# Optimization experiments

Measured on AMD Instinct MI355X. Metric: run time of the kernel, lower is better.

## Reference

```python
import jax, jax.numpy as jnp
import numpy as np

EMB = 768
HEADS = 8
HEAD_DIM = EMB // HEADS
SCALE = HEAD_DIM ** -0.5


def setup_inputs() -> dict:
    key = jax.random.key(0)
    ks = jax.random.split(key, 9)
    s = EMB ** -0.5
    return {
        "x": jax.random.normal(ks[0], (2, 4096, EMB), dtype=jnp.float32),
        "Wq": jax.random.normal(ks[1], (EMB, EMB), dtype=jnp.float32) * s,
        "bq": jax.random.normal(ks[2], (EMB,), dtype=jnp.float32) * 0.02,
        "Wk": jax.random.normal(ks[3], (EMB, EMB), dtype=jnp.float32) * s,
        "bk": jax.random.normal(ks[4], (EMB,), dtype=jnp.float32) * 0.02,
        "Wv": jax.random.normal(ks[5], (EMB, EMB), dtype=jnp.float32) * s,
        "bv": jax.random.normal(ks[6], (EMB,), dtype=jnp.float32) * 0.02,
        "Wo": jax.random.normal(ks[7], (EMB, EMB), dtype=jnp.float32) * s,
        "bo": jax.random.normal(ks[8], (EMB,), dtype=jnp.float32) * 0.02,
    }


def reference(x, Wq, bq, Wk, bk, Wv, bv, Wo, bo):
    b, n, _ = x.shape
    def split_heads(t):  # [b, n, emb] -> [b, h, n, d]
        return t.reshape(b, n, HEADS, HEAD_DIM).transpose(0, 2, 1, 3)
    q = split_heads(x @ Wq + bq)
    k = split_heads(x @ Wk + bk)
    v = split_heads(x @ Wv + bv)
    scores = jnp.einsum('bhqd,bhkd->bhqk', q, k)
    # NOTE: faithful to source — softmax first, THEN multiply by scale.
    attn = jax.nn.softmax(scores, axis=-1) * SCALE
    out = jnp.einsum('bhqk,bhkd->bhqd', attn, v)
    out = out.transpose(0, 2, 1, 3).reshape(b, n, EMB)
    return out @ Wo + bo
```

## Files before the change

### kernel.cpp

```cpp
#include <hip/hip_runtime.h>
#include <hip/hip_fp16.h>


typedef _Float16 half8 __attribute__((ext_vector_type(8)));
typedef _Float16 half4 __attribute__((ext_vector_type(4)));
typedef float   float4_ __attribute__((ext_vector_type(4)));
typedef float   f32x16 __attribute__((ext_vector_type(16)));

#define SCALE 0.102062072615966f
#define LOG2E 1.44269504088896340736f

__device__ __forceinline__ float4_ mfma16(half8 a, half8 b, float4_ c) {
    return __builtin_amdgcn_mfma_f32_16x16x32_f16(a, b, c, 0, 0, 0);
}
__device__ __forceinline__ f32x16 mfma32(half8 a, half8 b, f32x16 c) {
    return __builtin_amdgcn_mfma_f32_32x32x16_f16(a, b, c, 0, 0, 0);
}
__device__ __forceinline__ void gload16(const _Float16* g, _Float16* l) {
    __builtin_amdgcn_global_load_lds(
        (const __attribute__((address_space(1))) void*)g,
        (__attribute__((address_space(3))) void*)l, 16, 0, 0);
}


__global__ void cast_x(const float* __restrict__ x, _Float16* __restrict__ xb) {
    int i = blockIdx.x * 256 + threadIdx.x;
    float4_ v = ((const float4_*)x)[i];
    half4 h = { (_Float16)v[0], (_Float16)v[1], (_Float16)v[2], (_Float16)v[3] };
    ((half4*)xb)[i] = h;
}

__global__ void prep_w(const float* __restrict__ Wq, const float* __restrict__ Wk,
                       const float* __restrict__ Wv, const float* __restrict__ Wo,
                       _Float16* __restrict__ wqkv, _Float16* __restrict__ wot) {
    __shared__ float tile[64][65];
    const int bid = blockIdx.x;
    const int mat = bid / 144, rem = bid % 144;
    const int kt = rem / 12, ct = rem % 12;
    const float* W = (mat == 0) ? Wq : (mat == 1) ? Wk : (mat == 2) ? Wv : Wo;
    const int k0 = kt * 64, c0 = ct * 64;
    const int t = threadIdx.x;
    const int lr = t >> 4, lc = (t & 15) * 4;
    #pragma unroll
    for (int i = 0; i < 4; ++i) {
        float4_ v = *(const float4_*)(W + (size_t)(k0 + i * 16 + lr) * 768 + c0 + lc);
        tile[i * 16 + lr][lc + 0] = v[0];
        tile[i * 16 + lr][lc + 1] = v[1];
        tile[i * 16 + lr][lc + 2] = v[2];
        tile[i * 16 + lr][lc + 3] = v[3];
    }
    __syncthreads();
    const int cr = t >> 2, kq = (t & 3) * 16;
    _Float16* dst = (mat < 3) ? (wqkv + ((size_t)(mat * 768 + c0 + cr)) * 768 + k0 + kq)
                              : (wot  + ((size_t)(c0 + cr)) * 768 + k0 + kq);
    half8 h0, h1;
    #pragma unroll
    for (int j = 0; j < 8; ++j) {
        h0[j] = (_Float16)tile[kq + j][cr];
        h1[j] = (_Float16)tile[kq + 8 + j][cr];
    }
    *(half8*)dst = h0;
    *(half8*)(dst + 8) = h1;
}

__global__ void prep_bias(const float* __restrict__ bq, const float* __restrict__ bk,
                          const float* __restrict__ bv, float* __restrict__ bqkv) {
    int i = blockIdx.x * 256 + threadIdx.x;
    float v = (i < 768) ? bq[i] : (i < 1536) ? bk[i - 768] : bv[i - 1536];
    bqkv[i] = v;
}

__global__ __launch_bounds__(256, 2) void gemm_kernel(
    const _Float16* __restrict__ A, const _Float16* __restrict__ Bt,
    const float* __restrict__ bias, int mode,
    _Float16* __restrict__ Qo, _Float16* __restrict__ Ko, _Float16* __restrict__ Vto,
    float* __restrict__ out)
{
    __shared__ alignas(16) _Float16 Af[16 * 512];
    __shared__ alignas(16) _Float16 Bf[16 * 512];
    const int tid = threadIdx.x;
    const int lane = tid & 63, w = tid >> 6;
    const int wm = w >> 1, wn = w & 1;
    const int l15 = lane & 15, l4 = lane >> 4;
    const int m0 = blockIdx.y * 128;
    const int n0 = blockIdx.x * 128;

    const _Float16* gs[8];
    _Float16* ld[8];
    #pragma unroll
    for (int i = 0; i < 8; ++i) {
        int f = (w & 1) * 8 + i;
        int rg = f >> 1, kc = f & 1;
        int r0 = ((w < 2) ? m0 : n0) + rg * 16;
        gs[i] = ((w < 2) ? A : Bt) + (size_t)(r0 + l15) * 768 + kc * 32 + l4 * 8;
        ld[i] = ((w < 2) ? Af : Bf) + f * 512;
    }

    float4_ acc[4][4] = {};

    for (int k0 = 0; k0 < 768; k0 += 64) {
        #pragma unroll
        for (int i = 0; i < 8; ++i)
            gload16(gs[i] + k0, ld[i]);
        __syncthreads();
        #pragma unroll
        for (int kc = 0; kc < 2; ++kc) {
            half8 bfr[4];
            #pragma unroll
            for (int nt = 0; nt < 4; ++nt)
                bfr[nt] = *(const half8*)(Bf + (size_t)(((wn * 4 + nt) * 2 + kc) * 512 + lane * 8));
            #pragma unroll
            for (int mt = 0; mt < 4; ++mt) {
                half8 afr = *(const half8*)(Af + (size_t)(((wm * 4 + mt) * 2 + kc) * 512 + lane * 8));
                #pragma unroll
                for (int nt = 0; nt < 4; ++nt)
                    acc[mt][nt] = mfma16(afr, bfr[nt], acc[mt][nt]);
            }
        }
        __syncthreads();
    }

    #pragma unroll
    for (int mt = 0; mt < 4; ++mt)
    #pragma unroll
    for (int nt = 0; nt < 4; ++nt) {
        int gc = n0 + wn * 64 + nt * 16 + l15;
        float bv_ = bias[gc];
        #pragma unroll
        for (int r = 0; r < 4; ++r) {
            int gm = m0 + wm * 64 + mt * 16 + l4 * 4 + r;
            float val = acc[mt][nt][r] + bv_;
            if (mode == 1) {
                out[(size_t)gm * 768 + gc] = val;
            } else {
                int b = gm >> 12, n = gm & 4095;
                if (gc < 768) {
                    int h = gc / 96, d = gc % 96;
                    Qo[(((size_t)(b * 8 + h)) * 4096 + n) * 96 + d] = (_Float16)(val * LOG2E);
                } else if (gc < 1536) {
                    int c = gc - 768, h = c / 96, d = c % 96;
                    int bh = b * 8 + h;
                    size_t idx = (((size_t)bh * 128 + (n >> 5)) * 6 + (d >> 4)) * 512
                               + (size_t)((d >> 3) & 1) * 256 + (size_t)(n & 31) * 8 + (d & 7);
                    Ko[idx] = (_Float16)val;
                } else {
                    int c = gc - 1536, h = c / 96, d = c % 96;
                    int bh = b * 8 + h;
                    size_t idx = (((size_t)bh * 64 + (n >> 6)) * 12 + ((n >> 4) & 3) * 3 + (d >> 5)) * 512
                               + (size_t)((n >> 3) & 1) * 256 + (size_t)(d & 31) * 8 + (n & 7);
                    Vto[idx] = (_Float16)val;
                }
            }
        }
    }
}

__global__ __launch_bounds__(256, 2) void attn_kernel(
    const _Float16* __restrict__ Q, const _Float16* __restrict__ Kf,
    const _Float16* __restrict__ Vf, _Float16* __restrict__ AO)
{
    __shared__ alignas(16) _Float16 kvbuf[2][24 * 512];
    __shared__ float tab[4][32];

    const int tid = threadIdx.x;
    const int lane = tid & 63, w = tid >> 6;
    const int l31 = lane & 31, hi = lane >> 5;

    const int B = blockIdx.x;
    const int xcd = B & 7, j = B >> 3;
    const int bh = 2 * xcd + (j >> 5);
    const int qb = j & 31;
    const int q0 = qb * 128 + w * 32;

    const size_t qBase = (size_t)bh * 4096 * 96;
    const _Float16* kfb = Kf + (size_t)bh * 393216;
    const _Float16* vfb = Vf + (size_t)bh * 393216;

    half8 qf[6];
    #pragma unroll
    for (int dch = 0; dch < 6; ++dch)
        qf[dch] = *(const half8*)(Q + qBase + (size_t)(q0 + l31) * 96 + dch * 16 + hi * 8);

    f32x16 o0 = {}, o1 = {}, o2 = {};
    float m = -1e30f, l = 0.f;

    const int fbase = w * 6;
    const _Float16* gbase = ((fbase < 12) ? (kfb + (size_t)fbase * 512)
                                          : (vfb + (size_t)(fbase - 12) * 512)) + lane * 8;

    half8 streg[6], vreg[12];

    #pragma unroll
    for (int i = 0; i < 6; ++i)
        streg[i] = *(const half8*)(gbase + i * 512);
    #pragma unroll
    for (int i = 0; i < 6; ++i)
        *(half8*)(&kvbuf[0][(fbase + i) * 512 + lane * 8]) = streg[i];
    __syncthreads();

    int cur = 0;
    for (int t = 0; t < 64; ++t) {
        const int tn = (t + 1) & 63;
        #pragma unroll
        for (int i = 0; i < 6; ++i)
            streg[i] = *(const half8*)(gbase + (size_t)tn * 6144 + i * 512);

        const _Float16* kb = &kvbuf[cur][0];
        const _Float16* vb = &kvbuf[cur][12 * 512];

        f32x16 s0 = {}, s1 = {};
        __builtin_amdgcn_s_setprio(1);
        #pragma unroll
        for (int dch = 0; dch < 6; ++dch) {
            half8 k0 = *(const half8*)(kb + dch * 512 + lane * 8);
            half8 k1 = *(const half8*)(kb + (6 + dch) * 512 + lane * 8);
            s0 = mfma32(k0, qf[dch], s0);
            s1 = mfma32(k1, qf[dch], s1);
        }
        __builtin_amdgcn_s_setprio(0);

        #pragma unroll
        for (int i = 0; i < 12; ++i)
            vreg[i] = *(const half8*)(vb + i * 512 + lane * 8);

        float lm = fmaxf(s0[0], s0[1]);
        #pragma unroll
        for (int r = 2; r < 16; ++r) lm = fmaxf(lm, s0[r]);
        #pragma unroll
        for (int r = 0; r < 16; ++r) lm = fmaxf(lm, s1[r]);
        float pmax = fmaxf(lm, __shfl_xor(lm, 32));
        if (__any(pmax > m + 8.0f)) {
            float mn = fmaxf(m, pmax);
            float al = __builtin_exp2f(m - mn);
            m = mn; l *= al;
            if (hi == 0) tab[w][l31] = al;
            asm volatile("s_waitcnt lgkmcnt(0)" ::: "memory");
            #pragma unroll
            for (int r = 0; r < 16; ++r) {
                float alr = tab[w][(r & 3) + 8 * (r >> 2) + 4 * hi];
                o0[r] *= alr; o1[r] *= alr; o2[r] *= alr;
            }
        }
        float ls = 0.f;
        uint32_t Lp[16];
        #pragma unroll
        for (int kg = 0; kg < 2; ++kg) {
            const f32x16& s = kg ? s1 : s0;
            #pragma unroll
            for (int jg = 0; jg < 4; ++jg) {
                float p0 = __builtin_exp2f(s[4 * jg + 0] - m);
                float p1 = __builtin_exp2f(s[4 * jg + 1] - m);
                float p2 = __builtin_exp2f(s[4 * jg + 2] - m);
                float p3 = __builtin_exp2f(s[4 * jg + 3] - m);
                ls += (p0 + p1) + (p2 + p3);
                union { _Float16 h[2]; uint32_t u; } pk0, pk1;
                pk0.h[0] = (_Float16)p0; pk0.h[1] = (_Float16)p1;
                pk1.h[0] = (_Float16)p2; pk1.h[1] = (_Float16)p3;
                Lp[kg * 8 + jg * 2] = pk0.u; Lp[kg * 8 + jg * 2 + 1] = pk1.u;
            }
        }
        l += ls + __shfl_xor(ls, 32);

        half8 pa[4];
        #pragma unroll
        for (int kk = 0; kk < 4; ++kk) {
            uint32_t u0 = Lp[4 * kk], u1 = Lp[4 * kk + 1];
            uint32_t u2 = Lp[4 * kk + 2], u3 = Lp[4 * kk + 3];
            asm("v_permlane32_swap_b32 %0, %1" : "+v"(u0), "+v"(u2));
            asm("v_permlane32_swap_b32 %0, %1" : "+v"(u1), "+v"(u3));
            union { half8 h; uint32_t u[4]; } fr;
            fr.u[0] = u0; fr.u[1] = u1; fr.u[2] = u2; fr.u[3] = u3;
            pa[kk] = fr.h;
        }

        __builtin_amdgcn_s_setprio(1);
        #pragma unroll
        for (int kk = 0; kk < 4; ++kk) {
            o0 = mfma32(pa[kk], vreg[kk * 3 + 0], o0);
            o1 = mfma32(pa[kk], vreg[kk * 3 + 1], o1);
            o2 = mfma32(pa[kk], vreg[kk * 3 + 2], o2);
        }
        __builtin_amdgcn_s_setprio(0);

        __syncthreads();
        #pragma unroll
        for (int i = 0; i < 6; ++i)
            *(half8*)(&kvbuf[cur ^ 1][(fbase + i) * 512 + lane * 8]) = streg[i];
        __syncthreads();
        cur ^= 1;
    }

    if (hi == 0) tab[w][l31] = l;
    asm volatile("s_waitcnt lgkmcnt(0)" ::: "memory");
    const int b = bh >> 3, h = bh & 7;
    #pragma unroll
    for (int r = 0; r < 16; ++r) {
        int qrow = (r & 3) + 8 * (r >> 2) + 4 * hi;
        float inv = SCALE / tab[w][qrow];
        int n = q0 + qrow;
        size_t base = ((size_t)(b * 4096 + n)) * 768 + h * 96 + l31;
        AO[base]      = (_Float16)(o0[r] * inv);
        AO[base + 32] = (_Float16)(o1[r] * inv);
        AO[base + 64] = (_Float16)(o2[r] * inv);
    }
}


extern "C" void kernel_launch(void* const* d_in, const int* in_sizes, int n_in,
                              void* d_out, int out_size, void* d_ws, size_t ws_size,
                              hipStream_t stream) {
    const float* x  = (const float*)d_in[0];
    const float* Wq = (const float*)d_in[1];
    const float* bq = (const float*)d_in[2];
    const float* Wk = (const float*)d_in[3];
    const float* bk = (const float*)d_in[4];
    const float* Wv = (const float*)d_in[5];
    const float* bv = (const float*)d_in[6];
    const float* Wo = (const float*)d_in[7];
    const float* bo = (const float*)d_in[8];
    float* out = (float*)d_out;

    char* ws = (char*)d_ws;
    _Float16* xb   = (_Float16*)(ws);
    _Float16* wqkv = (_Float16*)(ws + 12582912);
    _Float16* wot  = (_Float16*)(ws + 16121856);
    float*    bqkv = (float*)   (ws + 17301504);
    _Float16* Qb   = (_Float16*)(ws + 17310720);
    _Float16* Kfb  = (_Float16*)(ws + 29893632);
    _Float16* Vfb  = (_Float16*)(ws + 42476544);
    _Float16* AO   = xb;

    cast_x<<<6144, 256, 0, stream>>>(x, xb);
    prep_w<<<576, 256, 0, stream>>>(Wq, Wk, Wv, Wo, wqkv, wot);
    prep_bias<<<9, 256, 0, stream>>>(bq, bk, bv, bqkv);

    gemm_kernel<<<dim3(18, 64), 256, 0, stream>>>(xb, wqkv, bqkv, 0, Qb, Kfb, Vfb, nullptr);

    attn_kernel<<<512, 256, 0, stream>>>(Qb, Kfb, Vfb, AO);

    gemm_kernel<<<dim3(6, 64), 256, 0, stream>>>(AO, wot, bo, 1, nullptr, nullptr, nullptr, out);
}
```

Measured before the change: 277.9 us.

## Load V fragments directly from global into registers, stage only K in LDS

V tiles are now fetched straight from global memory into per-wave registers, one tile ahead, instead of being cooperatively staged through shared memory. Only K is double-buffered in LDS, which halves LDS footprint and the per-iteration LDS store/load traffic. Each wave now reads the full V tile from global/L2 on its own, so V global traffic per block goes up fourfold, and the loads are issued late in the loop. The row-max reduction is also restructured into a tree to shorten the dependency chain.

```diff
diff --git a/kernel.cpp b/kernel.cpp
--- a/kernel.cpp
+++ b/kernel.cpp
@@ -159,7 +159,7 @@
     const _Float16* __restrict__ Q, const _Float16* __restrict__ Kf,
     const _Float16* __restrict__ Vf, _Float16* __restrict__ AO)
 {
-    __shared__ alignas(16) _Float16 kvbuf[2][24 * 512];
+    __shared__ alignas(16) _Float16 kbuf[2][12 * 512];
     __shared__ float tab[4][32];
 
     const int tid = threadIdx.x;
@@ -184,29 +184,31 @@
     f32x16 o0 = {}, o1 = {}, o2 = {};
     float m = -1e30f, l = 0.f;
 
-    const int fbase = w * 6;
-    const _Float16* gbase = ((fbase < 12) ? (kfb + (size_t)fbase * 512)
-                                          : (vfb + (size_t)(fbase - 12) * 512)) + lane * 8;
-
-    half8 streg[6], vreg[12];
-
-    #pragma unroll
-    for (int i = 0; i < 6; ++i)
-        streg[i] = *(const half8*)(gbase + i * 512);
-    #pragma unroll
-    for (int i = 0; i < 6; ++i)
-        *(half8*)(&kvbuf[0][(fbase + i) * 512 + lane * 8]) = streg[i];
+    const int fbase = w * 3;
+    const _Float16* gK = kfb + (size_t)fbase * 512 + lane * 8;
+    const _Float16* gV = vfb + lane * 8;
+
+    half8 streg[3], vreg[12];
+
+    #pragma unroll
+    for (int i = 0; i < 3; ++i)
+        streg[i] = *(const half8*)(gK + i * 512);
+    #pragma unroll
+    for (int i = 0; i < 12; ++i)
+        vreg[i] = *(const half8*)(gV + i * 512);
+    #pragma unroll
+    for (int i = 0; i < 3; ++i)
+        *(half8*)(&kbuf[0][(fbase + i) * 512 + lane * 8]) = streg[i];
     __syncthreads();
 
     int cur = 0;
     for (int t = 0; t < 64; ++t) {
         const int tn = (t + 1) & 63;
         #pragma unroll
-        for (int i = 0; i < 6; ++i)
-            streg[i] = *(const half8*)(gbase + (size_t)tn * 6144 + i * 512);
-
-        const _Float16* kb = &kvbuf[cur][0];
-        const _Float16* vb = &kvbuf[cur][12 * 512];
+        for (int i = 0; i < 3; ++i)
+            streg[i] = *(const half8*)(gK + (size_t)tn * 6144 + i * 512);
+
+        const _Float16* kb = &kbuf[cur][0];
 
         f32x16 s0 = {}, s1 = {};
         __builtin_amdgcn_s_setprio(1);
@@ -219,15 +221,13 @@
         }
         __builtin_amdgcn_s_setprio(0);
 
-        #pragma unroll
-        for (int i = 0; i < 12; ++i)
-            vreg[i] = *(const half8*)(vb + i * 512 + lane * 8);
-
-        float lm = fmaxf(s0[0], s0[1]);
-        #pragma unroll
-        for (int r = 2; r < 16; ++r) lm = fmaxf(lm, s0[r]);
-        #pragma unroll
-        for (int r = 0; r < 16; ++r) lm = fmaxf(lm, s1[r]);
+        float mx[8];
+        #pragma unroll
+        for (int r = 0; r < 8; ++r)
+            mx[r] = fmaxf(fmaxf(s0[r], s0[r + 8]), fmaxf(s1[r], s1[r + 8]));
+        mx[0] = fmaxf(mx[0], mx[4]); mx[1] = fmaxf(mx[1], mx[5]);
+        mx[2] = fmaxf(mx[2], mx[6]); mx[3] = fmaxf(mx[3], mx[7]);
+        float lm = fmaxf(fmaxf(mx[0], mx[1]), fmaxf(mx[2], mx[3]));
         float pmax = fmaxf(lm, __shfl_xor(lm, 32));
         if (__any(pmax > m + 8.0f)) {
             float mn = fmaxf(m, pmax);
@@ -282,10 +282,14 @@
         }
         __builtin_amdgcn_s_setprio(0);
 
+        #pragma unroll
+        for (int i = 0; i < 12; ++i)
+            vreg[i] = *(const half8*)(gV + ((size_t)tn * 12 + i) * 512);
+
         __syncthreads();
         #pragma unroll
-        for (int i = 0; i < 6; ++i)
-            *(half8*)(&kvbuf[cur ^ 1][(fbase + i) * 512 + lane * 8]) = streg[i];
+        for (int i = 0; i < 3; ++i)
+            *(half8*)(&kbuf[cur ^ 1][(fbase + i) * 512 + lane * 8]) = streg[i];
         __syncthreads();
         cur ^= 1;
     }
```

Measured after the change: 284.1 us. +2.2%, slower.
